# Performance work log

Hardware: AMD Instinct MI355X
Metric: run time of the kernel (lower is better)

## Reference

```python
import jax, jax.numpy as jnp
import numpy as np

B, N, C = 4, 2048, 1024


def setup_inputs() -> dict:
    key = jax.random.key(0)
    ks = jax.random.split(key, 5)
    s = 1.0 / np.sqrt(C)
    return {
        "event_f": jax.random.normal(ks[0], (B, N, C), dtype=jnp.float32),
        "img_f": jax.random.normal(ks[1], (B, N, C), dtype=jnp.float32),
        "Wq": jax.random.normal(ks[2], (C, C), dtype=jnp.float32) * s,
        "bq": jnp.zeros((C,), dtype=jnp.float32),
        "Wk": jax.random.normal(ks[3], (C, C), dtype=jnp.float32) * s,
        "bk": jnp.zeros((C,), dtype=jnp.float32),
        "Wv": jax.random.normal(ks[4], (C, C), dtype=jnp.float32) * s,
        "bv": jnp.zeros((C,), dtype=jnp.float32),
    }


def reference(event_f, img_f, Wq, bq, Wk, bk, Wv, bv):
    # pointwise projections (conv_query/key/val as 1x1 / Linear C->C)
    q = jnp.einsum("bnc,cd->bnd", event_f, Wq) + bq  # [B,N,C]
    k = jnp.einsum("bnc,cd->bnd", img_f, Wk) + bk
    v = jnp.einsum("bnc,cd->bnd", img_f, Wv) + bv
    scale = 1.0 / jnp.sqrt(jnp.asarray(q.shape[-1], dtype=q.dtype))
    scores = jnp.einsum("bqc,bkc->bqk", q, k) * scale  # [B,N,N]
    p_attn = jax.nn.softmax(scores, axis=-1)
    return jnp.einsum("bqk,bkc->bqc", p_attn, v)  # [B,N,C]
```

## Files before the change

kernel.cpp:

```cpp
#include <hip/hip_runtime.h>
#include <hip/hip_bf16.h>
#include <stdint.h>

typedef __bf16 bf16;
typedef __attribute__((ext_vector_type(8))) __bf16 bf16x8;
typedef __attribute__((ext_vector_type(4))) float f32x4;

typedef __attribute__((address_space(3))) char* lds_ptr;
typedef const __attribute__((address_space(1))) char* glb_ptr;

#define BZ 4
#define NN 2048
#define CC 1024

__device__ __forceinline__ void gload_lds16(const bf16* g, bf16* l) {
    __builtin_amdgcn_global_load_lds((glb_ptr)g, (lds_ptr)l, 16, 0, 0);
}

__device__ __forceinline__ void bar() {
    asm volatile("" ::: "memory");
    __builtin_amdgcn_s_barrier();
    asm volatile("" ::: "memory");
}

__global__ void cvt2_f32_bf16(const float* __restrict__ a, const float* __restrict__ b,
                              bf16* __restrict__ oa, bf16* __restrict__ ob, int n8) {
    int i = blockIdx.x * blockDim.x + threadIdx.x;
    if (i >= 2 * n8) return;
    const float4* p;
    bf16* dst;
    int j;
    if (i < n8) { p = (const float4*)a; dst = oa; j = i; }
    else        { p = (const float4*)b; dst = ob; j = i - n8; }
    float4 x = p[2 * j], y = p[2 * j + 1];
    bf16x8 o;
    o[0] = (bf16)x.x; o[1] = (bf16)x.y; o[2] = (bf16)x.z; o[3] = (bf16)x.w;
    o[4] = (bf16)y.x; o[5] = (bf16)y.y; o[6] = (bf16)y.z; o[7] = (bf16)y.w;
    *(bf16x8*)(dst + 8 * (size_t)j) = o;
}

__global__ void transposeW3(const float* __restrict__ W0, const float* __restrict__ W1,
                            const float* __restrict__ W2, bf16* __restrict__ T0,
                            bf16* __restrict__ T1, bf16* __restrict__ T2) {
    __shared__ bf16 t[32][33];
    const int z = blockIdx.z;
    const float* W = z == 0 ? W0 : (z == 1 ? W1 : W2);
    bf16* Wt = z == 0 ? T0 : (z == 1 ? T1 : T2);
    int d0 = blockIdx.x * 32, c0 = blockIdx.y * 32;
    int tx = threadIdx.x, ty = threadIdx.y;
#pragma unroll
    for (int i = 0; i < 4; i++)
        t[ty + 8 * i][tx] = (bf16)W[(size_t)(c0 + ty + 8 * i) * CC + d0 + tx];
    __syncthreads();
#pragma unroll
    for (int i = 0; i < 4; i++)
        Wt[(size_t)(d0 + ty + 8 * i) * CC + c0 + tx] = t[tx][ty + 8 * i];
}

__global__ void prep(const float* __restrict__ a, const float* __restrict__ b,
                     float* __restrict__ bqk, float* __restrict__ rowsum) {
    int i = blockIdx.x * blockDim.x + threadIdx.x;
    rowsum[i] = 0.f;
    if (i < CC) bqk[i] = a[i];
    else if (i < 2 * CC) bqk[i] = b[i - CC];
}


#define STAGE_A(kt_, hh_)                                                          \
    do {                                                                           \
        int _kt = (kt_);                                                           \
        if (_kt < nkt) {                                                           \
            const bf16* _s = gAs + (size_t)((hh_) * (BM / 2)) * lda +              \
                             (size_t)_kt * 64;                                     \
            bf16* _d = &LA[_kt & 1][((hh_) * (BM / 2) + wid * 16) * 64];           \
            gload_lds16(_s, _d);                                                   \
            gload_lds16(_s + (size_t)8 * lda, _d + 8 * 64);                        \
        }                                                                          \
    } while (0)

#define STAGE_B(kt_, hh_)                                                          \
    do {                                                                           \
        int _kt = (kt_);                                                           \
        if (_kt < nkt) {                                                           \
            const bf16* _s = gBs + (size_t)((hh_) * (BN / 2)) * ldb +              \
                             (size_t)_kt * 64;                                     \
            bf16* _d = &LB[_kt & 1][((hh_) * (BN / 2) + wid * 16) * 64];           \
            gload_lds16(_s, _d);                                                   \
            gload_lds16(_s + (size_t)8 * ldb, _d + 8 * 64);                        \
        }                                                                          \
    } while (0)

#define LDA_FRAG(buf_, mh_)                                                      \
    do {                                                                         \
        _Pragma("unroll") for (int _i = 0; _i < MI; ++_i)                        \
            _Pragma("unroll") for (int _ks = 0; _ks < 2; ++_ks)                  \
                a[_i][_ks] = *(const bf16x8*)&LA[buf_][                          \
                    (wm + (mh_) * (WAVE_M / 2) + _i * 16 + fr) * 64 +            \
                    (((_ks * 4 + hi) ^ lo) * 8)];                                \
    } while (0)

#define LDB_FRAG(buf_, nh_, dst_)                                                \
    do {                                                                         \
        _Pragma("unroll") for (int _j = 0; _j < 2; ++_j)                         \
            _Pragma("unroll") for (int _ks = 0; _ks < 2; ++_ks)                  \
                dst_[_j][_ks] = *(const bf16x8*)&LB[buf_][                       \
                    (wn + (nh_)*32 + _j * 16 + fr) * 64 +                        \
                    (((_ks * 4 + hi) ^ lo) * 8)];                                \
    } while (0)

#define MMQ(mh_, nh_, b_)                                                        \
    do {                                                                         \
        __builtin_amdgcn_s_setprio(1);                                           \
        _Pragma("unroll") for (int _i = 0; _i < MI; ++_i)                        \
            _Pragma("unroll") for (int _j = 0; _j < 2; ++_j)                     \
                _Pragma("unroll") for (int _ks = 0; _ks < 2; ++_ks)              \
                    acc[(mh_)*MI + _i][(nh_)*2 + _j] =                           \
                        __builtin_amdgcn_mfma_f32_16x16x32_bf16(                 \
                            a[_i][_ks], b_[_j][_ks],                             \
                            acc[(mh_)*MI + _i][(nh_)*2 + _j], 0, 0, 0);          \
        __builtin_amdgcn_s_setprio(0);                                           \
    } while (0)

#define VMW(n_) asm volatile("s_waitcnt vmcnt(" #n_ ")" ::: "memory")

template <int TB, int BM, int BN, int EPI, bool OUT_F32>
__global__ __launch_bounds__(TB, 2) void gemm8(
    const bf16* __restrict__ A, int lda,
    const bf16* __restrict__ Bt, int ldb,
    void* __restrict__ Cout, int ldc,
    float* __restrict__ aux, long long sAux, float scale,
    long long sA, long long sB, long long sC, int nkt) {
    constexpr int NW = TB / 64;
    constexpr int WNW = (TB == 512) ? 4 : 2;
    constexpr int WAVE_M = BM / 2;
    constexpr int MI = WAVE_M / 32;
    static_assert(BN / WNW == 64, "wave_n must be 64");
    __shared__ __align__(16) bf16 LA[2][BM * 64];
    __shared__ __align__(16) bf16 LB[2][BN * 64];

    const int nx = gridDim.x, ny = gridDim.y;
    const int nwg = nx * ny * gridDim.z;
    const int orig = blockIdx.x + nx * (blockIdx.y + ny * blockIdx.z);
    const int q = nwg >> 3, r = nwg & 7;
    const int xcd = orig & 7, land = orig >> 3;
    const int swz = (xcd < r ? xcd * (q + 1) : r * (q + 1) + (xcd - r) * q) + land;
    const int bx = swz % nx;
    const int tmp = swz / nx;
    const int by = tmp % ny, bz = tmp / ny;

    A += (size_t)bz * sA;
    Bt += (size_t)bz * sB;
    const int m0 = by * BM, n0 = bx * BN;
    const int t = threadIdx.x, wid = t >> 6, lane = t & 63;
    const int wm = (wid / WNW) * WAVE_M, wn = (wid % WNW) * 64;
    const int fr = lane & 15, hi = lane >> 4, lo = lane & 7;
    f32x4 acc[2 * MI][4] = {};

    const int srow = lane >> 3;
    const int schunk = lo ^ srow;
    const bf16* gAs = A + (size_t)(m0 + wid * 16 + srow) * lda + schunk * 8;
    const bf16* gBs = Bt + (size_t)(n0 + wid * 16 + srow) * ldb + schunk * 8;

    STAGE_A(0, 0); STAGE_A(0, 1); STAGE_B(0, 0); STAGE_B(0, 1);
    STAGE_B(1, 0); STAGE_A(1, 0); STAGE_B(1, 1);
    VMW(6);
    bar();

    bf16x8 a[MI][2], b0[2][2], b1[2][2];
    for (int kt = 0; kt < nkt; ++kt) {
        const int buf = kt & 1;
        LDA_FRAG(buf, 0);
        LDB_FRAG(buf, 0, b0);
        STAGE_A(kt + 1, 1);
        MMQ(0, 0, b0);
        bar();
        LDB_FRAG(buf, 1, b1);
        MMQ(0, 1, b1);
        bar();
        LDA_FRAG(buf, 1);
        STAGE_B(kt + 2, 0);
        MMQ(1, 1, b1);
        bar();
        STAGE_A(kt + 2, 0);
        STAGE_B(kt + 2, 1);
        MMQ(1, 0, b0);
        if (kt + 2 < nkt) VMW(6);
        else VMW(0);
        bar();
    }

    const int rq = hi * 4;
#pragma unroll
    for (int mh = 0; mh < 2; mh++)
#pragma unroll
        for (int i = 0; i < MI; i++) {
            const int row = m0 + wm + mh * (WAVE_M / 2) + i * 16 + rq;
            float rsum[4] = {0.f, 0.f, 0.f, 0.f};
            float inv[4];
            if (EPI == 4) {
#pragma unroll
                for (int rr = 0; rr < 4; rr++)
                    inv[rr] = 1.f / aux[bz * sAux + row + rr];
            }
#pragma unroll
            for (int nh = 0; nh < 2; nh++)
#pragma unroll
                for (int j = 0; j < 2; j++) {
                    int col = n0 + wn + nh * 32 + j * 16 + fr;
                    float bb = (EPI == 1) ? aux[bz * sAux + col] : 0.f;
                    f32x4 v = acc[mh * MI + i][nh * 2 + j];
#pragma unroll
                    for (int rr = 0; rr < 4; rr++) {
                        float o = v[rr] * scale + bb;
                        if (EPI == 2) o += aux[row + rr];
                        if (EPI == 3) { o = __expf(o - 6.f); rsum[rr] += o; }
                        if (EPI == 4) o *= inv[rr];
                        if (OUT_F32)
                            ((float*)Cout)[(size_t)bz * sC + (size_t)(row + rr) * ldc + col] = o;
                        else
                            ((bf16*)Cout)[(size_t)bz * sC + (size_t)(row + rr) * ldc + col] = (bf16)o;
                    }
                }
            if (EPI == 3) {
#pragma unroll
                for (int rr = 0; rr < 4; rr++) {
                    float s = rsum[rr];
                    s += __shfl_xor(s, 1);
                    s += __shfl_xor(s, 2);
                    s += __shfl_xor(s, 4);
                    s += __shfl_xor(s, 8);
                    if (fr == 0) atomicAdd(&aux[bz * sAux + row + rr], s);
                }
            }
        }
}

extern "C" void kernel_launch(void* const* d_in, const int* in_sizes, int n_in,
                              void* d_out, int out_size, void* d_ws, size_t ws_size,
                              hipStream_t stream) {
    const float* event_f = (const float*)d_in[0];
    const float* img_f   = (const float*)d_in[1];
    const float* Wq = (const float*)d_in[2];
    const float* bq = (const float*)d_in[3];
    const float* Wk = (const float*)d_in[4];
    const float* bk = (const float*)d_in[5];
    const float* Wv = (const float*)d_in[6];
    const float* bv = (const float*)d_in[7];
    float* out = (float*)d_out;

    bf16* ws = (bf16*)d_ws;
    const size_t MC = (size_t)BZ * NN * CC;
    const size_t CCsq = (size_t)CC * CC;
    bf16* Ebf  = ws;
    bf16* Ibf  = ws + MC;
    bf16* S    = ws;
    size_t off = 2 * MC;
    bf16* Wqkt = ws + off; off += 2 * CCsq;
    bf16* Wvt  = ws + off; off += CCsq;
    bf16* Qb   = ws + off; off += MC;
    bf16* Kb   = ws + off; off += MC;
    bf16* VT   = ws + off; off += MC;
    float* bqk = (float*)(ws + off);
    float* rowsum = bqk + 2 * CC;

    {
        int n8 = (int)(MC / 8);
        cvt2_f32_bf16<<<dim3((2 * n8 + 255) / 256), dim3(256), 0, stream>>>(
            event_f, img_f, Ebf, Ibf, n8);
    }
    transposeW3<<<dim3(CC / 32, CC / 32, 3), dim3(32, 8), 0, stream>>>(
        Wq, Wk, Wv, Wqkt, Wqkt + CCsq, Wvt);
    prep<<<dim3(BZ * NN / 256), dim3(256), 0, stream>>>(bq, bk, bqk, rowsum);
    gemm8<256, 128, 128, 1, false>
        <<<dim3(CC / 128, (BZ * NN) / 128, 2), dim3(256), 0, stream>>>(
        Ebf, CC, Wqkt, CC, Qb, CC, bqk, CC, 1.f,
        (long long)MC, (long long)CCsq, (long long)MC, CC / 64);
    gemm8<256, 128, 128, 2, false>
        <<<dim3(NN / 128, CC / 128, BZ), dim3(256), 0, stream>>>(
        Wvt, CC, Ibf, CC, VT, NN, (float*)bv, 0, 1.f,
        0, (long long)NN * CC, (long long)CC * NN, CC / 64);
    gemm8<512, 256, 256, 3, false>
        <<<dim3(NN / 256, NN / 256, BZ), dim3(512), 0, stream>>>(
        Qb, CC, Kb, CC, S, NN, rowsum, NN, 1.f / 32.f,
        (long long)NN * CC, (long long)NN * CC, (long long)NN * NN, CC / 64);
    gemm8<256, 128, 128, 4, true>
        <<<dim3(CC / 128, NN / 128, BZ), dim3(256), 0, stream>>>(
        S, NN, VT, NN, out, CC, rowsum, NN, 1.f,
        (long long)NN * NN, (long long)CC * NN, (long long)NN * CC, NN / 64);
}
```

Measured before the change: 167.5 us.

## Fold Wq·Wkᵀ into a single matrix to drop the key projection GEMM

Precomputes G = Wq·Wkᵀ with a split-K GEMM and a reduction kernel. Scores then become (E·G)·Iᵀ, so the separate Q and K projection GEMMs (two large B·N×C×C GEMMs) shrink to one, plus a small C×C×C GEMM. The query bias is kept as a per-key correction: u = Wk·bq feeds beta = img·u, computed inside the conversion kernel and added in the score epilogue. The key bias is dropped because it only adds a per-row constant, which softmax cancels. In exchange there are extra small kernels, atomics for beta, and extra bf16 rounding of the fused G matrix.

```diff
diff --git a/kernel.cpp b/kernel.cpp
--- a/kernel.cpp
+++ b/kernel.cpp
@@ -4,6 +4,7 @@
 
 typedef __bf16 bf16;
 typedef __attribute__((ext_vector_type(8))) __bf16 bf16x8;
+typedef __attribute__((ext_vector_type(4))) __bf16 bf16x4;
 typedef __attribute__((ext_vector_type(4))) float f32x4;
 
 typedef __attribute__((address_space(3))) char* lds_ptr;
@@ -23,29 +24,52 @@
     asm volatile("" ::: "memory");
 }
 
-__global__ void cvt2_f32_bf16(const float* __restrict__ a, const float* __restrict__ b,
-                              bf16* __restrict__ oa, bf16* __restrict__ ob, int n8) {
-    int i = blockIdx.x * blockDim.x + threadIdx.x;
-    if (i >= 2 * n8) return;
-    const float4* p;
+__global__ void ucomp(const float* __restrict__ Wk, const float* __restrict__ bq,
+                      float* __restrict__ u) {
+    __shared__ float red[4];
+    const int c = blockIdx.x, t = threadIdx.x;
+    float p = 0.f;
+    for (int d = t; d < CC; d += 256) p += Wk[(size_t)c * CC + d] * bq[d];
+#pragma unroll
+    for (int off = 32; off; off >>= 1) p += __shfl_xor(p, off);
+    if ((t & 63) == 0) red[t >> 6] = p;
+    __syncthreads();
+    if (t == 0) u[c] = red[0] + red[1] + red[2] + red[3];
+}
+
+__global__ void cvt4(const float* __restrict__ e, const float* __restrict__ im,
+                     const float* __restrict__ wq, const float* __restrict__ wk,
+                     bf16* __restrict__ oe, bf16* __restrict__ oi,
+                     bf16* __restrict__ owq, bf16* __restrict__ owk,
+                     const float* __restrict__ u, float* __restrict__ beta,
+                     int n8, int w8) {
+    int idx = blockIdx.x * blockDim.x + threadIdx.x;
+    const float* src;
     bf16* dst;
     int j;
-    if (i < n8) { p = (const float4*)a; dst = oa; j = i; }
-    else        { p = (const float4*)b; dst = ob; j = i - n8; }
-    float4 x = p[2 * j], y = p[2 * j + 1];
+    bool isI = false;
+    if (idx < n8) { src = e; dst = oe; j = idx; }
+    else if (idx < 2 * n8) { src = im; dst = oi; j = idx - n8; isI = true; }
+    else if (idx < 2 * n8 + w8) { src = wq; dst = owq; j = idx - 2 * n8; }
+    else if (idx < 2 * n8 + 2 * w8) { src = wk; dst = owk; j = idx - 2 * n8 - w8; }
+    else return;
+    float4 x = ((const float4*)src)[2 * j], y = ((const float4*)src)[2 * j + 1];
     bf16x8 o;
     o[0] = (bf16)x.x; o[1] = (bf16)x.y; o[2] = (bf16)x.z; o[3] = (bf16)x.w;
     o[4] = (bf16)y.x; o[5] = (bf16)y.y; o[6] = (bf16)y.z; o[7] = (bf16)y.w;
     *(bf16x8*)(dst + 8 * (size_t)j) = o;
-}
-
-__global__ void transposeW3(const float* __restrict__ W0, const float* __restrict__ W1,
-                            const float* __restrict__ W2, bf16* __restrict__ T0,
-                            bf16* __restrict__ T1, bf16* __restrict__ T2) {
+    if (isI) {
+        int c0 = (j & 127) * 8;
+        float p = x.x * u[c0] + x.y * u[c0 + 1] + x.z * u[c0 + 2] + x.w * u[c0 + 3] +
+                  y.x * u[c0 + 4] + y.y * u[c0 + 5] + y.z * u[c0 + 6] + y.w * u[c0 + 7];
+#pragma unroll
+        for (int off = 32; off; off >>= 1) p += __shfl_xor(p, off);
+        if ((threadIdx.x & 63) == 0) atomicAdd(&beta[j >> 7], p);
+    }
+}
+
+__global__ void transposeW1(const float* __restrict__ W, bf16* __restrict__ Wt) {
     __shared__ bf16 t[32][33];
-    const int z = blockIdx.z;
-    const float* W = z == 0 ? W0 : (z == 1 ? W1 : W2);
-    bf16* Wt = z == 0 ? T0 : (z == 1 ? T1 : T2);
     int d0 = blockIdx.x * 32, c0 = blockIdx.y * 32;
     int tx = threadIdx.x, ty = threadIdx.y;
 #pragma unroll
@@ -57,12 +81,20 @@
         Wt[(size_t)(d0 + ty + 8 * i) * CC + c0 + tx] = t[tx][ty + 8 * i];
 }
 
-__global__ void prep(const float* __restrict__ a, const float* __restrict__ b,
-                     float* __restrict__ bqk, float* __restrict__ rowsum) {
+__global__ void sumcvt(const float* __restrict__ P, bf16* __restrict__ G, int n4) {
     int i = blockIdx.x * blockDim.x + threadIdx.x;
-    rowsum[i] = 0.f;
-    if (i < CC) bqk[i] = a[i];
-    else if (i < 2 * CC) bqk[i] = b[i - CC];
+    if (i >= n4) return;
+    const size_t S1 = (size_t)CC * CC;
+    float4 a = ((const float4*)P)[i];
+    float4 b = ((const float4*)(P + S1))[i];
+    float4 c = ((const float4*)(P + 2 * S1))[i];
+    float4 d = ((const float4*)(P + 3 * S1))[i];
+    bf16x4 o;
+    o[0] = (bf16)(a.x + b.x + c.x + d.x);
+    o[1] = (bf16)(a.y + b.y + c.y + d.y);
+    o[2] = (bf16)(a.z + b.z + c.z + d.z);
+    o[3] = (bf16)(a.w + b.w + c.w + d.w);
+    *(bf16x4*)(G + 4 * (size_t)i) = o;
 }
 
 
@@ -128,9 +160,9 @@
     const bf16* __restrict__ A, int lda,
     const bf16* __restrict__ Bt, int ldb,
     void* __restrict__ Cout, int ldc,
-    float* __restrict__ aux, long long sAux, float scale,
+    float* __restrict__ aux, long long sAux,
+    const float* __restrict__ fold, long long sFold, float scale,
     long long sA, long long sB, long long sC, int nkt) {
-    constexpr int NW = TB / 64;
     constexpr int WNW = (TB == 512) ? 4 : 2;
     constexpr int WAVE_M = BM / 2;
     constexpr int MI = WAVE_M / 32;
@@ -207,13 +239,13 @@
 #pragma unroll
                 for (int j = 0; j < 2; j++) {
                     int col = n0 + wn + nh * 32 + j * 16 + fr;
-                    float bb = (EPI == 1) ? aux[bz * sAux + col] : 0.f;
+                    float fc = (EPI == 5) ? fold[bz * sFold + col] * scale : 0.f;
                     f32x4 v = acc[mh * MI + i][nh * 2 + j];
 #pragma unroll
                     for (int rr = 0; rr < 4; rr++) {
-                        float o = v[rr] * scale + bb;
+                        float o = v[rr] * scale;
                         if (EPI == 2) o += aux[row + rr];
-                        if (EPI == 3) { o = __expf(o - 6.f); rsum[rr] += o; }
+                        if (EPI == 5) { o = __expf(o + fc - 6.f); rsum[rr] += o; }
                         if (EPI == 4) o *= inv[rr];
                         if (OUT_F32)
                             ((float*)Cout)[(size_t)bz * sC + (size_t)(row + rr) * ldc + col] = o;
@@ -221,7 +253,7 @@
                             ((bf16*)Cout)[(size_t)bz * sC + (size_t)(row + rr) * ldc + col] = (bf16)o;
                     }
                 }
-            if (EPI == 3) {
+            if (EPI == 5) {
 #pragma unroll
                 for (int rr = 0; rr < 4; rr++) {
                     float s = rsum[rr];
@@ -247,44 +279,50 @@
     const float* Wv = (const float*)d_in[6];
     const float* bv = (const float*)d_in[7];
     float* out = (float*)d_out;
+    (void)bk;
 
     bf16* ws = (bf16*)d_ws;
     const size_t MC = (size_t)BZ * NN * CC;
     const size_t CCsq = (size_t)CC * CC;
     bf16* Ebf  = ws;
     bf16* Ibf  = ws + MC;
-    bf16* S    = ws;
     size_t off = 2 * MC;
-    bf16* Wqkt = ws + off; off += 2 * CCsq;
+    bf16* Wqbf = ws + off; off += CCsq;
+    bf16* Wkbf = ws + off; off += CCsq;
     bf16* Wvt  = ws + off; off += CCsq;
-    bf16* Qb   = ws + off; off += MC;
-    bf16* Kb   = ws + off; off += MC;
+    bf16* Gt   = ws + off; off += CCsq;
+    bf16* Tb   = ws + off; off += MC;
     bf16* VT   = ws + off; off += MC;
-    float* bqk = (float*)(ws + off);
-    float* rowsum = bqk + 2 * CC;
-
+    bf16* S    = ws + off; off += 2 * MC;
+    float* Gpart = (float*)S;
+    float* fbase  = (float*)(ws + off);
+    float* rowsum = fbase;
+    float* beta   = fbase + BZ * NN;
+    float* u      = fbase + 2 * BZ * NN;
+
+    hipMemsetAsync(rowsum, 0, 2 * BZ * NN * sizeof(float), stream);
+    ucomp<<<dim3(CC), dim3(256), 0, stream>>>(Wk, bq, u);
     {
-        int n8 = (int)(MC / 8);
-        cvt2_f32_bf16<<<dim3((2 * n8 + 255) / 256), dim3(256), 0, stream>>>(
-            event_f, img_f, Ebf, Ibf, n8);
+        int n8 = (int)(MC / 8), w8 = (int)(CCsq / 8);
+        int tot = 2 * n8 + 2 * w8;
+        cvt4<<<dim3((tot + 255) / 256), dim3(256), 0, stream>>>(
+            event_f, img_f, Wq, Wk, Ebf, Ibf, Wqbf, Wkbf, u, beta, n8, w8);
     }
-    transposeW3<<<dim3(CC / 32, CC / 32, 3), dim3(32, 8), 0, stream>>>(
-        Wq, Wk, Wv, Wqkt, Wqkt + CCsq, Wvt);
-    prep<<<dim3(BZ * NN / 256), dim3(256), 0, stream>>>(bq, bk, bqk, rowsum);
-    gemm8<256, 128, 128, 1, false>
-        <<<dim3(CC / 128, (BZ * NN) / 128, 2), dim3(256), 0, stream>>>(
-        Ebf, CC, Wqkt, CC, Qb, CC, bqk, CC, 1.f,
-        (long long)MC, (long long)CCsq, (long long)MC, CC / 64);
-    gemm8<256, 128, 128, 2, false>
-        <<<dim3(NN / 128, CC / 128, BZ), dim3(256), 0, stream>>>(
-        Wvt, CC, Ibf, CC, VT, NN, (float*)bv, 0, 1.f,
+    transposeW1<<<dim3(CC / 32, CC / 32), dim3(32, 8), 0, stream>>>(Wv, Wvt);
+    gemm8<256, 128, 128, 0, true><<<dim3(8, 8, 4), dim3(256), 0, stream>>>(
+        Wkbf, CC, Wqbf, CC, Gpart, CC, nullptr, 0, nullptr, 0, 1.f,
+        256, 256, (long long)CCsq, 4);
+    sumcvt<<<dim3((CCsq / 4 + 255) / 256), dim3(256), 0, stream>>>(
+        Gpart, Gt, (int)(CCsq / 4));
+    gemm8<256, 128, 128, 0, false><<<dim3(CC / 128, (BZ * NN) / 128, 1), dim3(256), 0, stream>>>(
+        Ebf, CC, Gt, CC, Tb, CC, nullptr, 0, nullptr, 0, 1.f, 0, 0, 0, CC / 64);
+    gemm8<256, 128, 128, 2, false><<<dim3(NN / 128, CC / 128, BZ), dim3(256), 0, stream>>>(
+        Wvt, CC, Ibf, CC, VT, NN, (float*)bv, 0, nullptr, 0, 1.f,
         0, (long long)NN * CC, (long long)CC * NN, CC / 64);
-    gemm8<512, 256, 256, 3, false>
-        <<<dim3(NN / 256, NN / 256, BZ), dim3(512), 0, stream>>>(
-        Qb, CC, Kb, CC, S, NN, rowsum, NN, 1.f / 32.f,
+    gemm8<512, 256, 256, 5, false><<<dim3(NN / 256, NN / 256, BZ), dim3(512), 0, stream>>>(
+        Tb, CC, Ibf, CC, S, NN, rowsum, NN, beta, NN, 1.f / 32.f,
         (long long)NN * CC, (long long)NN * CC, (long long)NN * NN, CC / 64);
-    gemm8<256, 128, 128, 4, true>
-        <<<dim3(CC / 128, NN / 128, BZ), dim3(256), 0, stream>>>(
-        S, NN, VT, NN, out, CC, rowsum, NN, 1.f,
+    gemm8<256, 128, 128, 4, true><<<dim3(CC / 128, NN / 128, BZ), dim3(256), 0, stream>>>(
+        S, NN, VT, NN, out, CC, rowsum, NN, nullptr, 0, 1.f,
         (long long)NN * NN, (long long)CC * NN, (long long)NN * CC, NN / 64);
 }
```

Result: no change. 168.9 us (+0.9%).
